# Kernel tuning notes

Measured on AMD Instinct MI355X. Metric: run time of the kernel, lower is better.

The kernel has to match this reference:

```python
import jax, jax.numpy as jnp
import numpy as np

C = 128          # feature_num
INHI_RANGE = C // 8 + 1   # 17, banded channel window width
HALF = INHI_RANGE // 2    # 8


def conv2d(x, w, b=None, pad=0):
    # x: [N,C,H,W], w: [O,I,kh,kw]
    y = jax.lax.conv_general_dilated(
        x, w, window_strides=(1, 1), padding=[(pad, pad), (pad, pad)],
        dimension_numbers=("NCHW", "OIHW", "NCHW"))
    if b is not None:
        y = y + b[None, :, None, None]
    return y


def maxpool(x, k, s, pad):
    # torch MaxPool2d pads with -inf
    return jax.lax.reduce_window(
        x, -jnp.inf, jax.lax.max,
        window_dimensions=(1, 1, k, k), window_strides=(1, 1, s, s),
        padding=[(0, 0), (0, 0), (pad, pad), (pad, pad)])


def lrn(x):
    # Banded cross-channel inhibition: for channel i, sum x^2 over channels
    # j in [i-HALF, i+HALF] (clamped). Original code does this as a dense
    # (128,C,C) bmm; here it is a windowed channel reduction via cumsum.
    # NOTE: the torch code detaches y (x.clone().detach()), so the
    # denominator is a constant w.r.t. autodiff -> stop_gradient.
    x2 = jax.lax.stop_gradient(x) ** 2                      # [N,C,H,W]
    cs = jnp.cumsum(x2, axis=1)
    cs = jnp.concatenate([jnp.zeros_like(cs[:, :1]), cs], axis=1)  # [N,C+1,H,W]
    idx = jnp.arange(C)
    hi = jnp.minimum(idx + HALF + 1, C)
    lo = jnp.maximum(idx - HALF, 0)
    y = cs[:, hi] - cs[:, lo]                               # windowed sum
    y = (y * (0.001 / INHI_RANGE) + 1.0) ** 0.75
    return x / y


def rcl(x, fw, fb, rw, iters=3):
    f = conv2d(x, fw, fb, pad=1)
    r = lrn(jax.nn.relu(f))
    for _ in range(iters):
        r = lrn(jax.nn.relu(f + conv2d(r, rw, None, pad=1)))
    return r


def setup_inputs() -> dict:
    key = jax.random.key(0)
    ks = jax.random.split(key, 20)
    d = {}
    d["x"] = jax.random.normal(ks[0], (128, 3, 64, 64), jnp.float32)
    d["conv1_w"] = jax.random.normal(ks[1], (C, 3, 5, 5), jnp.float32) * 0.05
    d["conv1_b"] = jnp.zeros((C,), jnp.float32)
    d["bn_g"] = jnp.ones((C,), jnp.float32)
    d["bn_b"] = jnp.zeros((C,), jnp.float32)
    for i, n in enumerate(["2", "3", "4", "5"]):
        d[f"f{n}_w"] = jax.random.normal(ks[2 + 3 * i], (C, C, 3, 3), jnp.float32) * 0.02
        d[f"f{n}_b"] = jnp.zeros((C,), jnp.float32)
        d[f"r{n}_w"] = jax.random.normal(ks[3 + 3 * i], (C, C, 3, 3), jnp.float32) * 0.02
    d["mlp_w"] = jax.random.normal(ks[18], (10, C), jnp.float32) * 0.05
    d["mlp_b"] = jnp.zeros((10,), jnp.float32)
    return d


def reference(x, conv1_w, conv1_b, bn_g, bn_b,
              f2_w, f2_b, r2_w, f3_w, f3_b, r3_w,
              f4_w, f4_b, r4_w, f5_w, f5_b, r5_w,
              mlp_w, mlp_b):
    h = conv2d(x, conv1_w, conv1_b, pad=2)                  # [128,C,64,64]
    # BatchNorm2d (training-mode batch statistics, eps=1e-5)
    mean = h.mean(axis=(0, 2, 3), keepdims=True)
    var = h.var(axis=(0, 2, 3), keepdims=True)
    h = (h - mean) * jax.lax.rsqrt(var + 1e-5)
    h = h * bn_g[None, :, None, None] + bn_b[None, :, None, None]
    h = jax.nn.relu(h)
    h = maxpool(h, 3, 2, 1)                                 # 64 -> 32
    h = rcl(h, f2_w, f2_b, r2_w)                            # dropout = identity (eval)
    h = rcl(h, f3_w, f3_b, r3_w)
    h = maxpool(h, 3, 2, 1)                                 # 32 -> 16
    h = rcl(h, f4_w, f4_b, r4_w)
    h = rcl(h, f5_w, f5_b, r5_w)
    h = maxpool(h, 3, 2, 0)                                 # 16 -> 7
    y = h.max(axis=(2, 3))                                  # global max pool [128,C]
    return y @ mlp_w.T + mlp_b
```

## Files before the change

kernel.cpp:

```cpp
#include <hip/hip_runtime.h>


#define CCH 128
constexpr float KAPPA = 0.001f / 17.0f;

typedef __attribute__((ext_vector_type(8))) _Float16 half8;
typedef __attribute__((ext_vector_type(4))) float f32x4;

union U4 { uint4 v; ushort us[8]; _Float16 h[8]; half8 f; };
union U2 { ushort4 u; _Float16 h[4]; };

__global__ __launch_bounds__(256) void zero_stats(float* __restrict__ s) {
    s[threadIdx.x] = 0.f;
}

__global__ __launch_bounds__(256) void wcvt1(const float* __restrict__ wsrc,
                                             _Float16* __restrict__ wdst)
{
    const int idx = blockIdx.x * 256 + threadIdx.x;
    const int kc = idx >> 12;
    const int rem = idx & 4095;
    const int co = rem >> 5;
    const int kk = rem & 31;
    const int k = kc * 32 + kk;
    wdst[idx] = (k < 75) ? (_Float16)wsrc[co * 75 + k] : (_Float16)0.f;
}

__global__ __launch_bounds__(256, 2) void conv1m(
    const float* __restrict__ x, const _Float16* __restrict__ wc1,
    const float* __restrict__ bias, float* __restrict__ stats,
    _Float16* __restrict__ ph, _Float16* __restrict__ pp)
{
    __shared__ _Float16 xst[3 * 8 * 68];
    __shared__ _Float16 bnc[4 * 64 * 128];
    __shared__ float ps[4][128], ps2[4][128];

    const int bid = blockIdx.x;
    const int n = bid & 127;
    const int strip = bid >> 7;
    const int y0 = strip * 4;
    const int tid = threadIdx.x;
    const int w = tid >> 6, l = tid & 63;
    const int l15 = l & 15, lg = l >> 4;

    const float* xn = x + (size_t)n * 3 * 4096;
    for (int i = tid; i < 3 * 8 * 68; i += 256) {
        int ci = i / (8 * 68);
        int rm = i - ci * (8 * 68);
        int r = rm / 68, c = rm - r * 68;
        int gy = y0 - 2 + r, gx = c - 2;
        float v = ((unsigned)gy < 64u && (unsigned)gx < 64u)
                      ? xn[ci * 4096 + gy * 64 + gx] : 0.f;
        xst[i] = (_Float16)v;
    }

    f32x4 acc[8][4];
    #pragma unroll
    for (int cot = 0; cot < 8; ++cot) {
        f32x4 bv = *(const f32x4*)&bias[cot * 16 + lg * 4];
        #pragma unroll
        for (int pt = 0; pt < 4; ++pt) acc[cot][pt] = bv;
    }
    __syncthreads();

    #pragma unroll
    for (int kc = 0; kc < 3; ++kc) {
        int ba[8];
        #pragma unroll
        for (int j = 0; j < 8; ++j) {
            int k = kc * 32 + lg * 8 + j;
            k = k > 74 ? 74 : k;
            int ci = k / 25;
            int r = k - ci * 25;
            int ky = r / 5;
            int kx = r - ky * 5;
            ba[j] = (ci * 8 + w + ky) * 68 + l15 + kx;
        }
        half8 bf[4];
        #pragma unroll
        for (int pt = 0; pt < 4; ++pt) {
            U4 bb;
            #pragma unroll
            for (int j = 0; j < 8; ++j) bb.h[j] = xst[ba[j] + pt * 16];
            bf[pt] = bb.f;
        }
        const _Float16* wk = wc1 + kc * 4096 + l15 * 32 + lg * 8;
        #pragma unroll
        for (int cot = 0; cot < 8; ++cot) {
            half8 av = *(const half8*)&wk[cot * 512];
            #pragma unroll
            for (int pt = 0; pt < 4; ++pt)
                acc[cot][pt] = __builtin_amdgcn_mfma_f32_16x16x32_f16(
                    av, bf[pt], acc[cot][pt], 0, 0, 0);
        }
    }

    #pragma unroll
    for (int cot = 0; cot < 8; ++cot) {
        float s[4] = {0.f, 0.f, 0.f, 0.f}, s2[4] = {0.f, 0.f, 0.f, 0.f};
        #pragma unroll
        for (int pt = 0; pt < 4; ++pt)
            #pragma unroll
            for (int j = 0; j < 4; ++j) {
                float v = acc[cot][pt][j];
                s[j] += v; s2[j] += v * v;
            }
        #pragma unroll
        for (int o = 1; o < 16; o <<= 1)
            #pragma unroll
            for (int j = 0; j < 4; ++j) {
                s[j]  += __shfl_xor(s[j], o, 64);
                s2[j] += __shfl_xor(s2[j], o, 64);
            }
        if (l15 == 0) {
            #pragma unroll
            for (int j = 0; j < 4; ++j) {
                ps[w][cot * 16 + lg * 4 + j] = s[j];
                ps2[w][cot * 16 + lg * 4 + j] = s2[j];
            }
        }
    }

    #pragma unroll
    for (int cot = 0; cot < 8; ++cot)
        #pragma unroll
        for (int pt = 0; pt < 4; ++pt) {
            int c = pt * 16 + l15;
            int colx = (cot * 16 + lg * 4) ^ ((c & 7) * 8);
            U2 pk;
            pk.h[0] = (_Float16)acc[cot][pt][0];
            pk.h[1] = (_Float16)acc[cot][pt][1];
            pk.h[2] = (_Float16)acc[cot][pt][2];
            pk.h[3] = (_Float16)acc[cot][pt][3];
            *(ushort4*)&bnc[(w * 64 + c) * 128 + colx] = pk.u;
        }
    __syncthreads();

    if (tid < 128) {
        float A = ps[0][tid] + ps[1][tid] + ps[2][tid] + ps[3][tid];
        float B = ps2[0][tid] + ps2[1][tid] + ps2[2][tid] + ps2[3][tid];
        atomicAdd(&stats[tid], A);
        atomicAdd(&stats[tid + 128], B);
    }

    constexpr float NEG = -3.0e38f;
    #pragma unroll
    for (int i = 0; i < 6; ++i) {
        int t = tid + i * 256;
        if (t < 1024) {
            int cg = t & 15, ox = (t >> 4) & 31, oysel = t >> 9;
            float m[8];
            #pragma unroll
            for (int j = 0; j < 8; ++j) m[j] = NEG;
            #pragma unroll
            for (int dy = 0; dy < 3; ++dy) {
                int r = 2 * oysel - 1 + dy;
                if (r < 0) continue;
                #pragma unroll
                for (int dx = 0; dx < 3; ++dx) {
                    int c = 2 * ox - 1 + dx;
                    if ((unsigned)c >= 64u) continue;
                    U4 v;
                    v.v = *(const uint4*)&bnc[(r * 64 + c) * 128 + ((cg * 8) ^ ((c & 7) * 8))];
                    #pragma unroll
                    for (int j = 0; j < 8; ++j) m[j] = fmaxf(m[j], (float)v.h[j]);
                }
            }
            U4 o;
            #pragma unroll
            for (int j = 0; j < 8; ++j) o.h[j] = (_Float16)m[j];
            int oy = strip * 2 + oysel;
            *(uint4*)&ph[((size_t)n * 1024 + oy * 32 + ox) * 128 + cg * 8] = o.v;
        } else if (strip < 15) {
            int t2 = t - 1024;
            int cg = t2 & 15, ox = (t2 >> 4) & 31;
            float m[8];
            #pragma unroll
            for (int j = 0; j < 8; ++j) m[j] = NEG;
            #pragma unroll
            for (int dx = 0; dx < 3; ++dx) {
                int c = 2 * ox - 1 + dx;
                if ((unsigned)c >= 64u) continue;
                U4 v;
                v.v = *(const uint4*)&bnc[(3 * 64 + c) * 128 + ((cg * 8) ^ ((c & 7) * 8))];
                #pragma unroll
                for (int j = 0; j < 8; ++j) m[j] = fmaxf(m[j], (float)v.h[j]);
            }
            U4 o;
            #pragma unroll
            for (int j = 0; j < 8; ++j) o.h[j] = (_Float16)m[j];
            *(uint4*)&pp[(((size_t)n * 15 + strip) * 32 + ox) * 128 + cg * 8] = o.v;
        }
    }
}

__global__ __launch_bounds__(256) void pool_fixr(const _Float16* __restrict__ pp,
                                                 _Float16* __restrict__ ph)
{
    const int idx = blockIdx.x * 256 + threadIdx.x;
    const int cg = idx & 15;
    const int ox = (idx >> 4) & 31;
    const int t = idx >> 9;
    const int s = t % 15;
    const int n = t / 15;
    const _Float16* p = pp + (((size_t)n * 15 + s) * 32 + ox) * 128 + cg * 8;
    _Float16* a = ph + ((size_t)n * 1024 + (2 * s + 2) * 32 + ox) * 128 + cg * 8;
    U4 av, bv;
    av.v = *(const uint4*)a;
    bv.v = *(const uint4*)p;
    #pragma unroll
    for (int j = 0; j < 8; ++j)
        if ((float)bv.h[j] > (float)av.h[j]) av.h[j] = bv.h[j];
    *(uint4*)a = av.v;
}

__global__ __launch_bounds__(128) void bn_finalize(
    const float* __restrict__ stats, const float* __restrict__ g,
    const float* __restrict__ b, float* __restrict__ scsh)
{
    const int c = threadIdx.x;
    const float M = 128.f * 4096.f;
    float mean = stats[c] / M;
    float var = stats[c + 128] / M - mean * mean;
    float rstd = rsqrtf(var + 1e-5f);
    float sc = g[c] * rstd;
    scsh[c] = sc;
    scsh[c + 128] = b[c] - mean * sc;
}

__global__ __launch_bounds__(256) void bnrelu(
    const _Float16* __restrict__ ph, const float* __restrict__ scsh,
    _Float16* __restrict__ out)
{
    const int idx = blockIdx.x * 256 + threadIdx.x;
    const int cg = idx & 15;
    const size_t e = (size_t)(idx >> 4) * 128 + cg * 8;
    U4 v; v.v = *(const uint4*)&ph[e];
    U4 o;
    #pragma unroll
    for (int j = 0; j < 8; ++j) {
        int co = cg * 8 + j;
        float f = (float)v.h[j] * scsh[co] + scsh[co + 128];
        o.h[j] = (_Float16)fmaxf(f, 0.f);
    }
    *(uint4*)&out[e] = o.v;
}

__global__ __launch_bounds__(256) void wcvt(const float* __restrict__ wsrc,
                                            _Float16* __restrict__ wdst)
{
    const int idx = blockIdx.x * 256 + threadIdx.x;
    const int t = idx >> 14;
    const int rem = idx & 16383;
    const int co = rem >> 7;
    const int ci = rem & 127;
    wdst[idx] = (_Float16)wsrc[(co * 128 + ci) * 9 + t];
}

template<int H, bool ADD_F>
__global__ __launch_bounds__(256, 2) void conv3f(
    const _Float16* __restrict__ in, const _Float16* __restrict__ wb,
    const float* __restrict__ bias, _Float16* __restrict__ fbuf,
    _Float16* __restrict__ outp)
{
    constexpr int W = H, HW = H * W;
    constexpr int XP = W + 2;
    constexpr int PITCH = 40;
    constexpr int ROWS = 10;
    constexpr int PTN = (H == 32) ? 4 : 2;
    constexpr int NPIX = PTN * 16;
    constexpr int STAGE = ROWS * XP * PITCH;
    constexpr int TASKS = ROWS * W * 4;
    constexpr int NIT = (TASKS + 255) / 256;
    constexpr int LOG4W = (H == 32) ? 7 : 6;
    constexpr int LDSH = 4 * NPIX * 128;

    __shared__ _Float16 xs[LDSH];

    const int bid = blockIdx.x;
    const int slot = bid >> 3;
    const int n = (bid & 7) + 8 * (slot & 15);
    const int y0 = (slot >> 4) * 8;
    const int tid = threadIdx.x;
    const int w = tid >> 6, l = tid & 63;
    const int l15 = l & 15, lg = l >> 4;

    for (int i = tid; i < STAGE / 2; i += 256) ((uint*)xs)[i] = 0;

    f32x4 acc[8][PTN];
    #pragma unroll
    for (int cot = 0; cot < 8; ++cot) {
        f32x4 bv = {0.f, 0.f, 0.f, 0.f};
        if constexpr (!ADD_F) bv = *(const f32x4*)&bias[cot * 16 + lg * 4];
        #pragma unroll
        for (int pt = 0; pt < PTN; ++pt) acc[cot][pt] = bv;
    }

    const _Float16* inb = in + (size_t)n * HW * 128;
    uint4 stg[NIT];

    auto issue = [&](int c0) {
        #pragma unroll
        for (int i = 0; i < NIT; ++i) {
            int t = tid + i * 256;
            uint4 v = {0u, 0u, 0u, 0u};
            if (TASKS % 256 == 0 || t < TASKS) {
                int g = t & 3, xx = (t >> 2) & (W - 1), yl = t >> LOG4W;
                int gy = y0 - 1 + yl;
                if ((unsigned)gy < (unsigned)H)
                    v = *(const uint4*)&inb[((size_t)(gy * W + xx)) * 128 + c0 + g * 8];
            }
            stg[i] = v;
        }
    };
    auto commit = [&]() {
        #pragma unroll
        for (int i = 0; i < NIT; ++i) {
            int t = tid + i * 256;
            if (TASKS % 256 == 0 || t < TASKS) {
                int g = t & 3, xx = (t >> 2) & (W - 1), yl = t >> LOG4W;
                *(uint4*)&xs[(yl * XP + xx + 1) * PITCH + g * 8] = stg[i];
            }
        }
    };

    int bofs[PTN];
    #pragma unroll
    for (int pt = 0; pt < PTN; ++pt) {
        int row_l = 2 * w + ((H == 32) ? (pt >> 1) : pt);
        int xb = ((H == 32) ? (pt & 1) * 16 : 0) + l15;
        bofs[pt] = ((row_l + 1) * XP + xb + 1) * PITCH + lg * 8;
    }
    const _Float16* wl = wb + l15 * 128 + lg * 8;

    issue(0);
    for (int cc = 0; cc < 4; ++cc) {
        const int c0 = cc * 32;
        __syncthreads();
        commit();
        if (cc < 3) issue(c0 + 32);
        __syncthreads();
        #pragma unroll
        for (int ky = -1; ky <= 1; ++ky)
            #pragma unroll
            for (int kx = -1; kx <= 1; ++kx) {
                const int t9 = (ky + 1) * 3 + (kx + 1);
                half8 bf[PTN];
                #pragma unroll
                for (int pt = 0; pt < PTN; ++pt)
                    bf[pt] = *(const half8*)&xs[bofs[pt] + (ky * XP + kx) * PITCH];
                const _Float16* wt = wl + t9 * 16384 + c0;
                #pragma unroll
                for (int coh = 0; coh < 2; ++coh) {
                    half8 av[4];
                    #pragma unroll
                    for (int j = 0; j < 4; ++j)
                        av[j] = *(const half8*)&wt[(coh * 4 + j) * 2048];
                    #pragma unroll
                    for (int j = 0; j < 4; ++j)
                        #pragma unroll
                        for (int pt = 0; pt < PTN; ++pt)
                            acc[coh * 4 + j][pt] = __builtin_amdgcn_mfma_f32_16x16x32_f16(
                                av[j], bf[pt], acc[coh * 4 + j][pt], 0, 0, 0);
                }
            }
    }

    __syncthreads();
    _Float16* bx = xs + w * (NPIX * 128);
    #pragma unroll
    for (int a = 0; a < 8; ++a)
        #pragma unroll
        for (int pt = 0; pt < PTN; ++pt) {
            const int wpx = pt * 16 + l15;
            const int col = (a * 16 + lg * 4) ^ ((wpx & 7) * 8);
            U2 pk;
            pk.h[0] = (_Float16)acc[a][pt][0];
            pk.h[1] = (_Float16)acc[a][pt][1];
            pk.h[2] = (_Float16)acc[a][pt][2];
            pk.h[3] = (_Float16)acc[a][pt][3];
            *(ushort4*)&bx[wpx * 128 + col] = pk.u;
        }
    __syncthreads();

    if (H == 32 || l < 32) {
        const int px = l & (NPIX - 1);
        const int p3 = px & 7;
        U4 sv[16];
        #pragma unroll
        for (int g = 0; g < 16; ++g)
            sv[g].v = *(const uint4*)&bx[px * 128 + ((g ^ p3) * 8)];

        const int row_l = 2 * w + ((H == 32) ? (px >> 5) : (px >> 4));
        const int xo = px & (W - 1);
        const size_t gbase = ((size_t)n * HW + (size_t)(y0 + row_l) * W + xo) * 128;

        if constexpr (ADD_F) {
            #pragma unroll
            for (int g = 0; g < 16; ++g) {
                U4 fv; fv.v = *(const uint4*)&fbuf[gbase + g * 8];
                #pragma unroll
                for (int j = 0; j < 8; ++j)
                    sv[g].h[j] = (_Float16)((float)sv[g].h[j] + (float)fv.h[j]);
            }
        } else {
            #pragma unroll
            for (int g = 0; g < 16; ++g)
                *(uint4*)&fbuf[gbase + g * 8] = sv[g].v;
        }

        float ring[17], zr[9], wsum = 0.f;
        #pragma unroll
        for (int i = 0; i < 17; ++i) ring[i] = 0.f;
        #pragma unroll
        for (int i = 0; i < 9; ++i) zr[i] = 0.f;
        U4 ob;
        #pragma unroll
        for (int c = 0; c < 136; ++c) {
            float z = 0.f;
            if (c < 128) {
                float v = (float)sv[c >> 3].h[c & 7];
                z = v > 0.f ? v : 0.f;
            }
            float zz = z * z;
            wsum += zz - ring[c % 17];
            ring[c % 17] = zz;
            zr[c % 9] = z;
            if (c >= 8) {
                int o = c - 8;
                float p75 = exp2f(-0.75f * log2f(wsum * KAPPA + 1.f));
                ob.h[o & 7] = (_Float16)(zr[(c + 1) % 9] * p75);
                if ((o & 7) == 7) *(uint4*)&outp[gbase + (o & ~7)] = ob.v;
            }
        }
    }
}

__global__ __launch_bounds__(256) void pool32v(const _Float16* __restrict__ in,
                                               _Float16* __restrict__ out)
{
    const int idx = blockIdx.x * 256 + threadIdx.x;
    const int cg = idx & 15;
    const int opix = (idx >> 4) & 255;
    const int n = idx >> 12;
    const int oy = opix >> 4, ox = opix & 15;
    const _Float16* ib = in + (size_t)n * 1024 * 128 + cg * 8;
    float m[8] = {0.f, 0.f, 0.f, 0.f, 0.f, 0.f, 0.f, 0.f};
    #pragma unroll
    for (int dy = -1; dy <= 1; ++dy) {
        int iy = 2 * oy + dy;
        if ((unsigned)iy >= 32u) continue;
        #pragma unroll
        for (int dx = -1; dx <= 1; ++dx) {
            int ix = 2 * ox + dx;
            if ((unsigned)ix >= 32u) continue;
            U4 v; v.v = *(const uint4*)&ib[(size_t)(iy * 32 + ix) * 128];
            #pragma unroll
            for (int i = 0; i < 8; ++i) m[i] = fmaxf(m[i], (float)v.h[i]);
        }
    }
    U4 o;
    #pragma unroll
    for (int i = 0; i < 8; ++i) o.h[i] = (_Float16)m[i];
    *(uint4*)&out[((size_t)n * 256 + opix) * 128 + cg * 8] = o.v;
}

__global__ __launch_bounds__(256) void gmax2(const _Float16* __restrict__ in,
                                             float* __restrict__ g)
{
    const int idx = blockIdx.x * 256 + threadIdx.x;
    const int c8 = idx & 15;
    const int n = idx >> 4;
    const _Float16* ib = in + (size_t)n * 256 * 128 + c8 * 8;
    float m[8] = {0.f, 0.f, 0.f, 0.f, 0.f, 0.f, 0.f, 0.f};
    for (int y = 0; y < 15; ++y)
        #pragma unroll
        for (int x = 0; x < 15; ++x) {
            U4 v; v.v = *(const uint4*)&ib[(size_t)(y * 16 + x) * 128];
            #pragma unroll
            for (int i = 0; i < 8; ++i) m[i] = fmaxf(m[i], (float)v.h[i]);
        }
    float* gb = g + n * 128 + c8 * 8;
    *(float4*)&gb[0] = {m[0], m[1], m[2], m[3]};
    *(float4*)&gb[4] = {m[4], m[5], m[6], m[7]};
}

__global__ __launch_bounds__(256) void mlp_k(
    const float* __restrict__ g, const float* __restrict__ w,
    const float* __restrict__ b, float* __restrict__ out)
{
    const int idx = blockIdx.x * 256 + threadIdx.x;
    if (idx >= 1280) return;
    const int n = idx / 10, k = idx - n * 10;
    float acc = b[k];
    for (int c = 0; c < CCH; ++c) acc += g[n * CCH + c] * w[k * CCH + c];
    out[idx] = acc;
}

extern "C" void kernel_launch(void* const* d_in, const int* in_sizes, int n_in,
                              void* d_out, int out_size, void* d_ws, size_t ws_size,
                              hipStream_t stream)
{
    const float* x   = (const float*)d_in[0];
    const float* w1  = (const float*)d_in[1];
    const float* b1  = (const float*)d_in[2];
    const float* bng = (const float*)d_in[3];
    const float* bnb = (const float*)d_in[4];
    const float* fw[4] = {(const float*)d_in[5],  (const float*)d_in[8],
                          (const float*)d_in[11], (const float*)d_in[14]};
    const float* fb[4] = {(const float*)d_in[6],  (const float*)d_in[9],
                          (const float*)d_in[12], (const float*)d_in[15]};
    const float* rw[4] = {(const float*)d_in[7],  (const float*)d_in[10],
                          (const float*)d_in[13], (const float*)d_in[16]};
    const float* mw = (const float*)d_in[17];
    const float* mb = (const float*)d_in[18];
    float* out = (float*)d_out;

    _Float16* ws16 = (_Float16*)d_ws;
    _Float16* buf0 = ws16;
    _Float16* buf1 = ws16 + 16777216;
    _Float16* Fb32 = ws16 + 2 * 16777216;
    _Float16* base3 = ws16 + 3 * 16777216;
    _Float16* A16a = base3;
    _Float16* A16b = base3 + 4194304;
    _Float16* F16  = base3 + 2 * 4194304;
    _Float16* Wb   = base3 + 3 * 4194304;
    float* stats = (float*)(Wb + 8 * 147456);
    float* scsh  = stats + 256;
    float* gm    = scsh + 256;
    _Float16* Pp  = (_Float16*)(gm + 16384);
    _Float16* Wc1 = Pp + 7864320;
    _Float16* PH  = buf1;

    zero_stats<<<1, 256, 0, stream>>>(stats);
    wcvt1<<<48, 256, 0, stream>>>(w1, Wc1);
    conv1m<<<2048, 256, 0, stream>>>(x, Wc1, b1, stats, PH, Pp);
    pool_fixr<<<3840, 256, 0, stream>>>(Pp, PH);
    bn_finalize<<<1, 128, 0, stream>>>(stats, bng, bnb, scsh);
    bnrelu<<<8192, 256, 0, stream>>>(PH, scsh, buf0);

    const float* lw[8] = {fw[0], rw[0], fw[1], rw[1], fw[2], rw[2], fw[3], rw[3]};
    for (int i = 0; i < 8; ++i)
        wcvt<<<576, 256, 0, stream>>>(lw[i], Wb + i * 147456);

    _Float16* cur = buf0;
    _Float16* alt = buf1;
    for (int s = 0; s < 2; ++s) {
        conv3f<32, false><<<512, 256, 0, stream>>>(cur, Wb + (2*s) * 147456, fb[s], Fb32, alt);
        { _Float16* t = cur; cur = alt; alt = t; }
        for (int it = 0; it < 3; ++it) {
            conv3f<32, true><<<512, 256, 0, stream>>>(cur, Wb + (2*s+1) * 147456, nullptr, Fb32, alt);
            { _Float16* t = cur; cur = alt; alt = t; }
        }
    }
    pool32v<<<2048, 256, 0, stream>>>(cur, A16a);

    _Float16* cur16 = A16a;
    _Float16* alt16 = A16b;
    for (int s = 2; s < 4; ++s) {
        conv3f<16, false><<<256, 256, 0, stream>>>(cur16, Wb + (2*s) * 147456, fb[s], F16, alt16);
        { _Float16* t = cur16; cur16 = alt16; alt16 = t; }
        for (int it = 0; it < 3; ++it) {
            conv3f<16, true><<<256, 256, 0, stream>>>(cur16, Wb + (2*s+1) * 147456, nullptr, F16, alt16);
            { _Float16* t = cur16; cur16 = alt16; alt16 = t; }
        }
    }
    gmax2<<<8, 256, 0, stream>>>(cur16, gm);
    mlp_k<<<5, 256, 0, stream>>>(gm, mw, mb, out);
}
```

Baseline: 1.386 ms.

## Halve conv3f row tile and split LRN epilogue across all lanes by channel segments

Each conv3f block now covers 4 output rows instead of 8 (ROWS 10→6), doubling the grid so more blocks run on the GPU. The LRN epilogue previously left half the lanes idle at H=16. It now splits the 128 channels into per-lane segments with an 8-channel halo on each side, so every lane of the wavefront does work. The cost is more halo rows staged per block, redundant halo LRN computation, and the same weights reloaded by twice as many blocks.

```diff
diff --git a/kernel.cpp b/kernel.cpp
--- a/kernel.cpp
+++ b/kernel.cpp
@@ -266,21 +266,25 @@
     constexpr int W = H, HW = H * W;
     constexpr int XP = W + 2;
     constexpr int PITCH = 40;
-    constexpr int ROWS = 10;
-    constexpr int PTN = (H == 32) ? 4 : 2;
-    constexpr int NPIX = PTN * 16;
+    constexpr int ROWS = 6;
+    constexpr int PTN = W / 16;
+    constexpr int NPIX = W;
     constexpr int STAGE = ROWS * XP * PITCH;
     constexpr int TASKS = ROWS * W * 4;
     constexpr int NIT = (TASKS + 255) / 256;
     constexpr int LOG4W = (H == 32) ? 7 : 6;
     constexpr int LDSH = 4 * NPIX * 128;
+    constexpr int NSUB = 64 / NPIX;
+    constexpr int SEGO = 128 / NSUB;
+    constexpr int LEN = SEGO + 16;
+    constexpr int NSV = LEN / 8;
 
     __shared__ _Float16 xs[LDSH];
 
     const int bid = blockIdx.x;
     const int slot = bid >> 3;
     const int n = (bid & 7) + 8 * (slot & 15);
-    const int y0 = (slot >> 4) * 8;
+    const int y0 = (slot >> 4) * 4;
     const int tid = threadIdx.x;
     const int w = tid >> 6, l = tid & 63;
     const int l15 = l & 15, lg = l >> 4;
@@ -326,11 +330,8 @@
 
     int bofs[PTN];
     #pragma unroll
-    for (int pt = 0; pt < PTN; ++pt) {
-        int row_l = 2 * w + ((H == 32) ? (pt >> 1) : pt);
-        int xb = ((H == 32) ? (pt & 1) * 16 : 0) + l15;
-        bofs[pt] = ((row_l + 1) * XP + xb + 1) * PITCH + lg * 8;
-    }
+    for (int pt = 0; pt < PTN; ++pt)
+        bofs[pt] = ((w + 1) * XP + pt * 16 + l15 + 1) * PITCH + lg * 8;
     const _Float16* wl = wb + l15 * 128 + lg * 8;
 
     issue(0);
@@ -383,54 +384,60 @@
         }
     __syncthreads();
 
-    if (H == 32 || l < 32) {
-        const int px = l & (NPIX - 1);
-        const int p3 = px & 7;
-        U4 sv[16];
-        #pragma unroll
-        for (int g = 0; g < 16; ++g)
-            sv[g].v = *(const uint4*)&bx[px * 128 + ((g ^ p3) * 8)];
-
-        const int row_l = 2 * w + ((H == 32) ? (px >> 5) : (px >> 4));
-        const int xo = px & (W - 1);
-        const size_t gbase = ((size_t)n * HW + (size_t)(y0 + row_l) * W + xo) * 128;
-
-        if constexpr (ADD_F) {
-            #pragma unroll
-            for (int g = 0; g < 16; ++g) {
-                U4 fv; fv.v = *(const uint4*)&fbuf[gbase + g * 8];
-                #pragma unroll
-                for (int j = 0; j < 8; ++j)
-                    sv[g].h[j] = (_Float16)((float)sv[g].h[j] + (float)fv.h[j]);
-            }
-        } else {
-            #pragma unroll
-            for (int g = 0; g < 16; ++g)
-                *(uint4*)&fbuf[gbase + g * 8] = sv[g].v;
-        }
-
-        float ring[17], zr[9], wsum = 0.f;
-        #pragma unroll
-        for (int i = 0; i < 17; ++i) ring[i] = 0.f;
-        #pragma unroll
-        for (int i = 0; i < 9; ++i) zr[i] = 0.f;
-        U4 ob;
-        #pragma unroll
-        for (int c = 0; c < 136; ++c) {
-            float z = 0.f;
-            if (c < 128) {
-                float v = (float)sv[c >> 3].h[c & 7];
-                z = v > 0.f ? v : 0.f;
-            }
-            float zz = z * z;
-            wsum += zz - ring[c % 17];
-            ring[c % 17] = zz;
-            zr[c % 9] = z;
-            if (c >= 8) {
-                int o = c - 8;
-                float p75 = exp2f(-0.75f * log2f(wsum * KAPPA + 1.f));
-                ob.h[o & 7] = (_Float16)(zr[(c + 1) % 9] * p75);
-                if ((o & 7) == 7) *(uint4*)&outp[gbase + (o & ~7)] = ob.v;
+    const int px = l & (NPIX - 1);
+    const int sub = l >> ((H == 32) ? 5 : 4);
+    const int p3 = px & 7;
+    const int cstart = sub ? (SEGO * sub - 8) : 0;
+    const int gb0 = cstart >> 3;
+    const int zlim = 128 - cstart;
+    const int wlo = sub ? 16 : 8;
+    const int whi = wlo + SEGO;
+
+    U4 sv[NSV];
+    #pragma unroll
+    for (int i = 0; i < NSV; ++i) {
+        int g = gb0 + i; g = g > 15 ? 15 : g;
+        sv[i].v = *(const uint4*)&bx[px * 128 + ((g ^ p3) * 8)];
+    }
+
+    const size_t gbase = ((size_t)n * HW + (size_t)(y0 + w) * W + px) * 128;
+
+    if constexpr (ADD_F) {
+        #pragma unroll
+        for (int i = 0; i < NSV; ++i) {
+            int g = gb0 + i; g = g > 15 ? 15 : g;
+            U4 fv; fv.v = *(const uint4*)&fbuf[gbase + g * 8];
+            #pragma unroll
+            for (int j = 0; j < 8; ++j)
+                sv[i].h[j] = (_Float16)((float)sv[i].h[j] + (float)fv.h[j]);
+        }
+    }
+
+    float ring[17], zr[9], wsum = 0.f;
+    #pragma unroll
+    for (int i = 0; i < 17; ++i) ring[i] = 0.f;
+    #pragma unroll
+    for (int i = 0; i < 9; ++i) zr[i] = 0.f;
+    U4 ob;
+    #pragma unroll
+    for (int cl = 0; cl < LEN; ++cl) {
+        float v = (float)sv[cl >> 3].h[cl & 7];
+        float z = (cl < zlim && v > 0.f) ? v : 0.f;
+        float zz = z * z;
+        wsum += zz - ring[cl % 17];
+        ring[cl % 17] = zz;
+        zr[cl % 9] = z;
+        if (cl >= 8) {
+            const int q = (cl - 8) & 7;
+            float p75 = exp2f(-0.75f * log2f(wsum * KAPPA + 1.f));
+            ob.h[q] = (_Float16)(zr[(cl + 1) % 9] * p75);
+            if (q == 7) {
+                if (cl >= wlo && cl < whi) {
+                    const int o = cstart + cl - 8;
+                    *(uint4*)&outp[gbase + (o & ~7)] = ob.v;
+                    if constexpr (!ADD_F)
+                        *(uint4*)&fbuf[gbase + (o & ~7)] = sv[(cl - 8) >> 3].v;
+                }
             }
         }
     }
@@ -546,10 +553,10 @@
     _Float16* cur = buf0;
     _Float16* alt = buf1;
     for (int s = 0; s < 2; ++s) {
-        conv3f<32, false><<<512, 256, 0, stream>>>(cur, Wb + (2*s) * 147456, fb[s], Fb32, alt);
+        conv3f<32, false><<<1024, 256, 0, stream>>>(cur, Wb + (2*s) * 147456, fb[s], Fb32, alt);
         { _Float16* t = cur; cur = alt; alt = t; }
         for (int it = 0; it < 3; ++it) {
-            conv3f<32, true><<<512, 256, 0, stream>>>(cur, Wb + (2*s+1) * 147456, nullptr, Fb32, alt);
+            conv3f<32, true><<<1024, 256, 0, stream>>>(cur, Wb + (2*s+1) * 147456, nullptr, Fb32, alt);
             { _Float16* t = cur; cur = alt; alt = t; }
         }
     }
@@ -558,10 +565,10 @@
     _Float16* cur16 = A16a;
     _Float16* alt16 = A16b;
     for (int s = 2; s < 4; ++s) {
-        conv3f<16, false><<<256, 256, 0, stream>>>(cur16, Wb + (2*s) * 147456, fb[s], F16, alt16);
+        conv3f<16, false><<<512, 256, 0, stream>>>(cur16, Wb + (2*s) * 147456, fb[s], F16, alt16);
         { _Float16* t = cur16; cur16 = alt16; alt16 = t; }
         for (int it = 0; it < 3; ++it) {
-            conv3f<16, true><<<256, 256, 0, stream>>>(cur16, Wb + (2*s+1) * 147456, nullptr, F16, alt16);
+            conv3f<16, true><<<512, 256, 0, stream>>>(cur16, Wb + (2*s+1) * 147456, nullptr, F16, alt16);
             { _Float16* t = cur16; cur16 = alt16; alt16 = t; }
         }
     }
```

Result: slower. 1.971 ms (+42.3%).

## Coalesce conv epilogue global I/O through LDS and prefetch residual f early

Applied to the files above, without the earlier changes.

The fused conv3+LRN epilogue used to read and write fbuf and outp with per-pixel strided 256-byte rows, one pixel per lane. It now stages data through the swizzled LDS tile so that each wavefront moves contiguous 16-byte chunks, and the residual f tile is prefetched into registers during the last channel chunk of the MFMA loop so its latency overlaps compute. The residual is added in the f32 accumulator domain before the fp16 write to LDS. The cost is more LDS traffic and syncthreads, plus extra registers for the prefetch, which may hurt occupancy at 2 blocks per CU.

```diff
diff --git a/kernel.cpp b/kernel.cpp
--- a/kernel.cpp
+++ b/kernel.cpp
@@ -274,6 +274,7 @@
     constexpr int NIT = (TASKS + 255) / 256;
     constexpr int LOG4W = (H == 32) ? 7 : 6;
     constexpr int LDSH = 4 * NPIX * 128;
+    constexpr int CPL = NPIX / 4;
 
     __shared__ _Float16 xs[LDSH];
 
@@ -297,7 +298,9 @@
     }
 
     const _Float16* inb = in + (size_t)n * HW * 128;
+    const size_t gw = ((size_t)n * HW + (size_t)(y0 + 2 * w) * W) * 128;
     uint4 stg[NIT];
+    uint4 freg[CPL];
 
     auto issue = [&](int c0) {
         #pragma unroll
@@ -339,6 +342,13 @@
         __syncthreads();
         commit();
         if (cc < 3) issue(c0 + 32);
+        if constexpr (ADD_F) {
+            if (cc == 3) {
+                #pragma unroll
+                for (int i = 0; i < CPL; ++i)
+                    freg[i] = *(const uint4*)&fbuf[gw + (size_t)(i * 64 + l) * 8];
+            }
+        }
         __syncthreads();
         #pragma unroll
         for (int ky = -1; ky <= 1; ++ky)
@@ -368,47 +378,68 @@
 
     __syncthreads();
     _Float16* bx = xs + w * (NPIX * 128);
-    #pragma unroll
-    for (int a = 0; a < 8; ++a)
-        #pragma unroll
-        for (int pt = 0; pt < PTN; ++pt) {
-            const int wpx = pt * 16 + l15;
-            const int col = (a * 16 + lg * 4) ^ ((wpx & 7) * 8);
-            U2 pk;
-            pk.h[0] = (_Float16)acc[a][pt][0];
-            pk.h[1] = (_Float16)acc[a][pt][1];
-            pk.h[2] = (_Float16)acc[a][pt][2];
-            pk.h[3] = (_Float16)acc[a][pt][3];
-            *(ushort4*)&bx[wpx * 128 + col] = pk.u;
-        }
+
+    if constexpr (ADD_F) {
+        #pragma unroll
+        for (int i = 0; i < CPL; ++i) {
+            int px = i * 4 + (l >> 4);
+            int col = ((l & 15) * 8) ^ ((px & 7) * 8);
+            *(uint4*)&bx[px * 128 + col] = freg[i];
+        }
+        __syncthreads();
+        #pragma unroll
+        for (int a = 0; a < 8; ++a)
+            #pragma unroll
+            for (int pt = 0; pt < PTN; ++pt) {
+                const int wpx = pt * 16 + l15;
+                const int col = (a * 16 + lg * 4) ^ ((wpx & 7) * 8);
+                U2 cur; cur.u = *(const ushort4*)&bx[wpx * 128 + col];
+                U2 pk;
+                pk.h[0] = (_Float16)(acc[a][pt][0] + (float)cur.h[0]);
+                pk.h[1] = (_Float16)(acc[a][pt][1] + (float)cur.h[1]);
+                pk.h[2] = (_Float16)(acc[a][pt][2] + (float)cur.h[2]);
+                pk.h[3] = (_Float16)(acc[a][pt][3] + (float)cur.h[3]);
+                *(ushort4*)&bx[wpx * 128 + col] = pk.u;
+            }
+    } else {
+        #pragma unroll
+        for (int a = 0; a < 8; ++a)
+            #pragma unroll
+            for (int pt = 0; pt < PTN; ++pt) {
+                const int wpx = pt * 16 + l15;
+                const int col = (a * 16 + lg * 4) ^ ((wpx & 7) * 8);
+                U2 pk;
+                pk.h[0] = (_Float16)acc[a][pt][0];
+                pk.h[1] = (_Float16)acc[a][pt][1];
+                pk.h[2] = (_Float16)acc[a][pt][2];
+                pk.h[3] = (_Float16)acc[a][pt][3];
+                *(ushort4*)&bx[wpx * 128 + col] = pk.u;
+            }
+    }
     __syncthreads();
 
-    if (H == 32 || l < 32) {
-        const int px = l & (NPIX - 1);
-        const int p3 = px & 7;
-        U4 sv[16];
+    if constexpr (!ADD_F) {
+        #pragma unroll
+        for (int i = 0; i < CPL; ++i) {
+            int px = i * 4 + (l >> 4);
+            int col = ((l & 15) * 8) ^ ((px & 7) * 8);
+            uint4 v = *(const uint4*)&bx[px * 128 + col];
+            *(uint4*)&fbuf[gw + (size_t)(i * 64 + l) * 8] = v;
+        }
+    }
+
+    const bool ractive = (H == 32) || (l < 32);
+    const int px = (H == 32) ? l : (l & 31);
+    const int p3 = px & 7;
+    U4 sv[16];
+    if (ractive) {
         #pragma unroll
         for (int g = 0; g < 16; ++g)
             sv[g].v = *(const uint4*)&bx[px * 128 + ((g ^ p3) * 8)];
-
-        const int row_l = 2 * w + ((H == 32) ? (px >> 5) : (px >> 4));
-        const int xo = px & (W - 1);
-        const size_t gbase = ((size_t)n * HW + (size_t)(y0 + row_l) * W + xo) * 128;
-
-        if constexpr (ADD_F) {
-            #pragma unroll
-            for (int g = 0; g < 16; ++g) {
-                U4 fv; fv.v = *(const uint4*)&fbuf[gbase + g * 8];
-                #pragma unroll
-                for (int j = 0; j < 8; ++j)
-                    sv[g].h[j] = (_Float16)((float)sv[g].h[j] + (float)fv.h[j]);
-            }
-        } else {
-            #pragma unroll
-            for (int g = 0; g < 16; ++g)
-                *(uint4*)&fbuf[gbase + g * 8] = sv[g].v;
-        }
-
+    }
+    __syncthreads();
+
+    if (ractive) {
         float ring[17], zr[9], wsum = 0.f;
         #pragma unroll
         for (int i = 0; i < 17; ++i) ring[i] = 0.f;
@@ -430,9 +461,19 @@
                 int o = c - 8;
                 float p75 = exp2f(-0.75f * log2f(wsum * KAPPA + 1.f));
                 ob.h[o & 7] = (_Float16)(zr[(c + 1) % 9] * p75);
-                if ((o & 7) == 7) *(uint4*)&outp[gbase + (o & ~7)] = ob.v;
-            }
-        }
+                if ((o & 7) == 7)
+                    *(uint4*)&bx[px * 128 + (((o >> 3) ^ p3) * 8)] = ob.v;
+            }
+        }
+    }
+    __syncthreads();
+
+    #pragma unroll
+    for (int i = 0; i < CPL; ++i) {
+        int px2 = i * 4 + (l >> 4);
+        int col = ((l & 15) * 8) ^ ((px2 & 7) * 8);
+        uint4 v = *(const uint4*)&bx[px2 * 128 + col];
+        *(uint4*)&outp[gw + (size_t)(i * 64 + l) * 8] = v;
     }
 }
 
```

After: 1.455 ms. 5.0% more time.

## Stage conv3f weights in LDS with register prefetch and single-wave occupancy

Applied to the files above, without the earlier changes.

The 3x3 conv kernel now copies each 32-channel slice of the weights for all 9 taps into shared memory (padded rows of 40 halves). It prefetches the next slice through registers alongside the input tile, so MFMA A-operands come from LDS instead of repeated global/L2 loads. The pipeline is restructured: the first slice is loaded before the loop, and each iteration commits the next slice and issues the one after it. The added LDS (about 92KB of weights) and 18 extra uint4 prefetch registers force launch bounds down to one block per SM, trading occupancy and latency hiding for weight reuse.

```diff
diff --git a/kernel.cpp b/kernel.cpp
--- a/kernel.cpp
+++ b/kernel.cpp
@@ -258,7 +258,7 @@
 }
 
 template<int H, bool ADD_F>
-__global__ __launch_bounds__(256, 2) void conv3f(
+__global__ __launch_bounds__(256, 1) void conv3f(
     const _Float16* __restrict__ in, const _Float16* __restrict__ wb,
     const float* __restrict__ bias, _Float16* __restrict__ fbuf,
     _Float16* __restrict__ outp)
@@ -269,11 +269,14 @@
     constexpr int ROWS = 10;
     constexpr int PTN = (H == 32) ? 4 : 2;
     constexpr int NPIX = PTN * 16;
+    constexpr int WROW = 40;
+    constexpr int WOFF = 9 * 128 * WROW;
     constexpr int STAGE = ROWS * XP * PITCH;
     constexpr int TASKS = ROWS * W * 4;
     constexpr int NIT = (TASKS + 255) / 256;
+    constexpr int WNIT = 18;
     constexpr int LOG4W = (H == 32) ? 7 : 6;
-    constexpr int LDSH = 4 * NPIX * 128;
+    constexpr int LDSH = WOFF + STAGE;
 
     __shared__ _Float16 xs[LDSH];
 
@@ -285,7 +288,7 @@
     const int w = tid >> 6, l = tid & 63;
     const int l15 = l & 15, lg = l >> 4;
 
-    for (int i = tid; i < STAGE / 2; i += 256) ((uint*)xs)[i] = 0;
+    for (int i = tid; i < STAGE / 2; i += 256) ((uint*)(xs + WOFF))[i] = 0;
 
     f32x4 acc[8][PTN];
     #pragma unroll
@@ -298,6 +301,7 @@
 
     const _Float16* inb = in + (size_t)n * HW * 128;
     uint4 stg[NIT];
+    uint4 wreg[WNIT];
 
     auto issue = [&](int c0) {
         #pragma unroll
@@ -319,8 +323,24 @@
             int t = tid + i * 256;
             if (TASKS % 256 == 0 || t < TASKS) {
                 int g = t & 3, xx = (t >> 2) & (W - 1), yl = t >> LOG4W;
-                *(uint4*)&xs[(yl * XP + xx + 1) * PITCH + g * 8] = stg[i];
-            }
+                *(uint4*)&xs[WOFF + (yl * XP + xx + 1) * PITCH + g * 8] = stg[i];
+            }
+        }
+    };
+    auto wissue = [&](int c0) {
+        #pragma unroll
+        for (int i = 0; i < WNIT; ++i) {
+            int tsk = tid + i * 256;
+            int g = tsk & 3, co = (tsk >> 2) & 127, tp = tsk >> 9;
+            wreg[i] = *(const uint4*)&wb[tp * 16384 + co * 128 + c0 + g * 8];
+        }
+    };
+    auto wcommit = [&]() {
+        #pragma unroll
+        for (int i = 0; i < WNIT; ++i) {
+            int tsk = tid + i * 256;
+            int g = tsk & 3, co = (tsk >> 2) & 127, tp = tsk >> 9;
+            *(uint4*)&xs[(tp * 128 + co) * WROW + g * 8] = wreg[i];
         }
     };
 
@@ -329,17 +349,20 @@
     for (int pt = 0; pt < PTN; ++pt) {
         int row_l = 2 * w + ((H == 32) ? (pt >> 1) : pt);
         int xb = ((H == 32) ? (pt & 1) * 16 : 0) + l15;
-        bofs[pt] = ((row_l + 1) * XP + xb + 1) * PITCH + lg * 8;
-    }
-    const _Float16* wl = wb + l15 * 128 + lg * 8;
+        bofs[pt] = WOFF + ((row_l + 1) * XP + xb + 1) * PITCH + lg * 8;
+    }
+    const int wlane = l15 * WROW + lg * 8;
 
     issue(0);
+    wissue(0);
+    __syncthreads();
+    commit();
+    wcommit();
+    issue(32);
+    wissue(32);
+    __syncthreads();
+
     for (int cc = 0; cc < 4; ++cc) {
-        const int c0 = cc * 32;
-        __syncthreads();
-        commit();
-        if (cc < 3) issue(c0 + 32);
-        __syncthreads();
         #pragma unroll
         for (int ky = -1; ky <= 1; ++ky)
             #pragma unroll
@@ -349,13 +372,13 @@
                 #pragma unroll
                 for (int pt = 0; pt < PTN; ++pt)
                     bf[pt] = *(const half8*)&xs[bofs[pt] + (ky * XP + kx) * PITCH];
-                const _Float16* wt = wl + t9 * 16384 + c0;
+                const int wbase = t9 * (128 * WROW) + wlane;
                 #pragma unroll
                 for (int coh = 0; coh < 2; ++coh) {
                     half8 av[4];
                     #pragma unroll
                     for (int j = 0; j < 4; ++j)
-                        av[j] = *(const half8*)&wt[(coh * 4 + j) * 2048];
+                        av[j] = *(const half8*)&xs[wbase + (coh * 4 + j) * (16 * WROW)];
                     #pragma unroll
                     for (int j = 0; j < 4; ++j)
                         #pragma unroll
@@ -364,6 +387,13 @@
                                 av[j], bf[pt], acc[coh * 4 + j][pt], 0, 0, 0);
                 }
             }
+        if (cc < 3) {
+            __syncthreads();
+            commit();
+            wcommit();
+            if (cc < 2) { issue((cc + 2) * 32); wissue((cc + 2) * 32); }
+            __syncthreads();
+        }
     }
 
     __syncthreads();
```

Measured after the change: 1.306 ms. 1.06x faster.
